# Kernel optimization log

Hardware: AMD Instinct MI355X
Metric: run time of the kernel (lower is better)

## Reference

```python
import jax, jax.numpy as jnp
import numpy as np

B, C, S = 32, 64, 112
RATIO = 8
EPS = 1e-5


def conv1x1(x, w, b):
    # 1x1 conv == channel-mixing matmul. x:[B,C,H,W], w:[O,C], b:[O]
    return jnp.einsum('oc,bchw->bohw', w, x) + b[None, :, None, None]


def dwconv(x, w, b):
    # grouped 1x1 conv with groups=C: per-channel scale + bias
    return x * w[None, :, None, None] + b[None, :, None, None]


def bn(x, g, b):
    # BatchNorm2d in training mode: batch stats over (N,H,W), biased var
    m = x.mean((0, 2, 3), keepdims=True)
    v = x.var((0, 2, 3), keepdims=True)
    return (x - m) * jax.lax.rsqrt(v + EPS) * g[None, :, None, None] + b[None, :, None, None]


def avgpool(x, k):
    # nn.AvgPool2d(k): kernel k, stride k, VALID (floor) padding
    s = jax.lax.reduce_window(x, 0.0, jax.lax.add, (1, 1, k, k), (1, 1, k, k), 'VALID')
    return s / float(k * k)


def setup_inputs() -> dict:
    key = jax.random.key(0)
    ks = jax.random.split(key, 20)
    C2, H = 2 * C, (2 * C) // RATIO

    def n(k, shape, s=0.02):
        return jax.random.normal(k, shape, jnp.float32) * s

    return {
        'rgb': jax.random.normal(ks[0], (B, C, S, S), jnp.float32),
        'fre': jax.random.normal(ks[1], (B, C, S, S), jnp.float32),
        'wq_fad': n(ks[2], (C, C)), 'bq_fad': jnp.zeros((C,), jnp.float32),
        'wq_lfs': n(ks[3], (C, C)), 'bq_lfs': jnp.zeros((C,), jnp.float32),
        'wk_fad': n(ks[4], (C, C)), 'bk_fad': jnp.zeros((C,), jnp.float32),
        'wk_lfs': n(ks[5], (C, C)), 'bk_lfs': jnp.zeros((C,), jnp.float32),
        'fad_gamma': n(ks[6], (1,), 1.0), 'lfs_gamma': n(ks[7], (1,), 1.0),
        'fad_cw': n(ks[8], (C,), 1.0), 'fad_cb': jnp.zeros((C,), jnp.float32),
        'fad_bg': jnp.ones((C,), jnp.float32), 'fad_bb': jnp.zeros((C,), jnp.float32),
        'lfs_cw': n(ks[9], (C,), 1.0), 'lfs_cb': jnp.zeros((C,), jnp.float32),
        'lfs_bg': jnp.ones((C,), jnp.float32), 'lfs_bb': jnp.zeros((C,), jnp.float32),
        'lin1_w': n(ks[10], (3,), 0.3), 'lin2_w': n(ks[11], (3,), 0.3),
        'mlp_w1': n(ks[12], (H, C2)), 'mlp_w2': n(ks[13], (C2, H)),
        'rgb_cw': n(ks[14], (C,), 1.0), 'rgb_cb': jnp.zeros((C,), jnp.float32),
        'rgb_bg': jnp.ones((C,), jnp.float32), 'rgb_bb': jnp.zeros((C,), jnp.float32),
        'fre_cw': n(ks[15], (C,), 1.0), 'fre_cb': jnp.zeros((C,), jnp.float32),
        'fre_bg': jnp.ones((C,), jnp.float32), 'fre_bb': jnp.zeros((C,), jnp.float32),
    }


def reference(rgb, fre, wq_fad, bq_fad, wq_lfs, bq_lfs, wk_fad, bk_fad, wk_lfs, bk_lfs,
              fad_gamma, lfs_gamma, fad_cw, fad_cb, fad_bg, fad_bb,
              lfs_cw, lfs_cb, lfs_bg, lfs_bb, lin1_w, lin2_w, mlp_w1, mlp_w2,
              rgb_cw, rgb_cb, rgb_bg, rgb_bb, fre_cw, fre_cb, fre_bg, fre_bb):
    Bn, Cn, Sz, _ = rgb.shape
    # ---- MixBlock: cross attention over folded (B*C) batch ----
    qF = conv1x1(rgb, wq_fad, bq_fad).reshape(Bn * Cn, Sz, Sz)
    qL = conv1x1(fre, wq_lfs, bq_lfs).reshape(Bn * Cn, Sz, Sz)
    Mq = jnp.concatenate([qF, qL], axis=2)          # [BC, S, 2S]
    kF = conv1x1(rgb, wk_fad, bk_fad).reshape(Bn * Cn, Sz, Sz).transpose(0, 2, 1)
    kL = conv1x1(fre, wk_lfs, bk_lfs).reshape(Bn * Cn, Sz, Sz).transpose(0, 2, 1)
    Mk = jnp.concatenate([kF, kL], axis=1)          # [BC, 2S, S]
    attn = jax.nn.softmax(jnp.matmul(Mq, Mk), axis=-1).reshape(Bn, Cn, Sz, Sz)
    att_lfs = fre * attn * (jax.nn.sigmoid(lfs_gamma) * 2.0 - 1.0)
    y_fad = rgb + bn(dwconv(att_lfs, fad_cw, fad_cb), fad_bg, fad_bb)
    att_fad = rgb * attn * (jax.nn.sigmoid(fad_gamma) * 2.0 - 1.0)
    y_lfs = fre + bn(dwconv(att_fad, lfs_cw, lfs_cb), lfs_bg, lfs_bb)
    # ---- MSCA on concatenated channels ----
    x = jnp.concatenate([y_fad, y_lfs], axis=1)     # [B, 2C, S, S]
    avgs, maxs = [], []
    for k in (3, 5, 7):
        m = avgpool(x, k)
        avgs.append(m.mean((2, 3)))
        maxs.append(m.max((2, 3)))
    a_p = jnp.stack(avgs, -1) @ lin1_w              # [B, 2C]
    m_p = jnp.stack(maxs, -1) @ lin2_w

    def mlp(v):
        h = jax.nn.relu(jnp.einsum('rc,bc->br', mlp_w1, v))
        return jnp.einsum('cr,br->bc', mlp_w2, h)

    ca = jax.nn.sigmoid(mlp(a_p) + mlp(m_p))        # [B, 2C]
    r_c = ca[:, :Cn, None, None]
    f_c = ca[:, Cn:, None, None]
    rgb_out = y_fad + bn(dwconv(r_c * y_fad, rgb_cw, rgb_cb), rgb_bg, rgb_bb)
    fre_out = y_lfs + bn(dwconv(f_c * y_lfs, fre_cw, fre_cb), fre_bg, fre_bb)
    return (rgb_out, fre_out)
```

## Files before the change

kernel.cpp:

```cpp
#include <hip/hip_runtime.h>
#include <hip/hip_bf16.h>
#include <stdint.h>

#define NE 25690112ull
#define PP 12544
#define SS 112
#define EPSV 1e-5f

typedef __attribute__((ext_vector_type(8))) short short8v;
typedef __attribute__((ext_vector_type(4))) float float4v;

__device__ __forceinline__ unsigned short f2bf(float x){
  union { float f; uint32_t u; } v; v.f = x;
  uint32_t r = (v.u + 0x7fffu + ((v.u >> 16) & 1u)) >> 16;
  return (unsigned short)r;
}
__device__ __forceinline__ float bf2f(unsigned short u){ return __uint_as_float(((uint32_t)u) << 16); }

__global__ __launch_bounds__(256) void k1_conv(
    const float* __restrict__ rgb, const float* __restrict__ fre,
    const float* __restrict__ wq_fad, const float* __restrict__ bq_fad,
    const float* __restrict__ wk_fad, const float* __restrict__ bk_fad,
    const float* __restrict__ wq_lfs, const float* __restrict__ bq_lfs,
    const float* __restrict__ wk_lfs, const float* __restrict__ bk_lfs,
    unsigned short* __restrict__ qF, unsigned short* __restrict__ kF,
    unsigned short* __restrict__ qL, unsigned short* __restrict__ kL)
{
  const int bx = blockIdx.x, b = blockIdx.y, z = blockIdx.z;
  const float* X  = z ? fre : rgb;
  const float* Wq = z ? wq_lfs : wq_fad;
  const float* Bq = z ? bq_lfs : bq_fad;
  const float* Wk = z ? wk_lfs : wk_fad;
  const float* Bk = z ? bk_lfs : bk_fad;
  unsigned short* Oq = z ? qL : qF;
  unsigned short* Ok = z ? kL : kF;

  const int tid = threadIdx.x, lane = tid & 63, w = tid >> 6;
  const int lc = lane & 15, l4 = lane >> 4;

  short8v wqf[4][2], wkf[4][2];
  float bq[4], bk[4];
  #pragma unroll
  for (int ot = 0; ot < 4; ++ot){
    bq[ot] = Bq[ot*16 + lc];
    bk[ot] = Bk[ot*16 + lc];
    #pragma unroll
    for (int ks = 0; ks < 2; ++ks){
      const int base = (ot*16 + lc)*64 + ks*32 + l4*8;
      const float4 q0 = *(const float4*)(Wq + base);
      const float4 q1 = *(const float4*)(Wq + base + 4);
      const float4 k0 = *(const float4*)(Wk + base);
      const float4 k1 = *(const float4*)(Wk + base + 4);
      short8v vq, vk;
      vq[0]=(short)f2bf(q0.x); vq[1]=(short)f2bf(q0.y); vq[2]=(short)f2bf(q0.z); vq[3]=(short)f2bf(q0.w);
      vq[4]=(short)f2bf(q1.x); vq[5]=(short)f2bf(q1.y); vq[6]=(short)f2bf(q1.z); vq[7]=(short)f2bf(q1.w);
      vk[0]=(short)f2bf(k0.x); vk[1]=(short)f2bf(k0.y); vk[2]=(short)f2bf(k0.z); vk[3]=(short)f2bf(k0.w);
      vk[4]=(short)f2bf(k1.x); vk[5]=(short)f2bf(k1.y); vk[6]=(short)f2bf(k1.z); vk[7]=(short)f2bf(k1.w);
      wqf[ot][ks] = vq; wkf[ot][ks] = vk;
    }
  }

  const size_t xbase = (size_t)b * 64 * PP;
  #pragma unroll
  for (int t = 0; t < 4; ++t){
    const int p0 = bx*256 + (t*4 + w)*16;
    float af[2][8];
    #pragma unroll
    for (int ks = 0; ks < 2; ++ks)
      #pragma unroll
      for (int j = 0; j < 8; ++j)
        af[ks][j] = X[xbase + (size_t)(ks*32 + l4*8 + j)*PP + p0 + lc];
    short8v a0, a1;
    #pragma unroll
    for (int j = 0; j < 8; ++j){ a0[j] = (short)f2bf(af[0][j]); a1[j] = (short)f2bf(af[1][j]); }

    float4v aq[4], ak[4];
    #pragma unroll
    for (int ot = 0; ot < 4; ++ot){
      aq[ot] = (float4v){bq[ot], bq[ot], bq[ot], bq[ot]};
      ak[ot] = (float4v){bk[ot], bk[ot], bk[ot], bk[ot]};
    }
    #pragma unroll
    for (int ot = 0; ot < 4; ++ot){
      aq[ot] = __builtin_amdgcn_mfma_f32_16x16x32_bf16(a0, wqf[ot][0], aq[ot], 0, 0, 0);
      aq[ot] = __builtin_amdgcn_mfma_f32_16x16x32_bf16(a1, wqf[ot][1], aq[ot], 0, 0, 0);
      ak[ot] = __builtin_amdgcn_mfma_f32_16x16x32_bf16(a0, wkf[ot][0], ak[ot], 0, 0, 0);
      ak[ot] = __builtin_amdgcn_mfma_f32_16x16x32_bf16(a1, wkf[ot][1], ak[ot], 0, 0, 0);
    }
    #pragma unroll
    for (int ot = 0; ot < 4; ++ot){
      const size_t off = ((size_t)b*64 + ot*16 + lc)*PP + p0 + l4*4;
      ushort4 sq, sk;
      sq.x = f2bf(aq[ot][0]); sq.y = f2bf(aq[ot][1]); sq.z = f2bf(aq[ot][2]); sq.w = f2bf(aq[ot][3]);
      sk.x = f2bf(ak[ot][0]); sk.y = f2bf(ak[ot][1]); sk.z = f2bf(ak[ot][2]); sk.w = f2bf(ak[ot][3]);
      *(ushort4*)(Oq + off) = sq;
      *(ushort4*)(Ok + off) = sk;
    }
  }
}

__global__ __launch_bounds__(448) void k2_attn(
    unsigned short* __restrict__ qF, const unsigned short* __restrict__ qL,
    const unsigned short* __restrict__ kF, const unsigned short* __restrict__ kL,
    const float* __restrict__ rgb, const float* __restrict__ fre,
    const float* __restrict__ fad_gamma, const float* __restrict__ lfs_gamma,
    float* __restrict__ stats)
{
  const int bc = blockIdx.x, c = bc & 63;
  const size_t plane = (size_t)bc * PP;
  __shared__ __align__(16) unsigned short ksF[112][128];
  __shared__ __align__(16) unsigned short ksL[112][128];
  const int tid = threadIdx.x, lane = tid & 63, w = tid >> 6;
  const int l4 = lane >> 4, lc = lane & 15;

  const uint32_t* kFu = (const uint32_t*)kF + plane/2;
  const uint32_t* kLu = (const uint32_t*)kL + plane/2;
  for (int i = tid; i < 7168; i += 448){
    int row = i >> 6, wd = i & 63;
    uint32_t vF = (wd < 56) ? kFu[row*56 + wd] : 0u;
    uint32_t vL = (wd < 56) ? kLu[row*56 + wd] : 0u;
    uint32_t byteS = (uint32_t)((row << 8) | (wd << 2)) ^ (uint32_t)((row & 7) << 4);
    *(uint32_t*)((char*)&ksF[0][0] + byteS) = vF;
    *(uint32_t*)((char*)&ksL[0][0] + byteS) = vL;
  }
  __syncthreads();

  float4v acc[7];
  #pragma unroll
  for (int ct = 0; ct < 7; ++ct) acc[ct] = (float4v)0.f;

  const unsigned short* qFp = qF + plane;
  const unsigned short* qLp = qL + plane;
  const int qrow = w*16 + lc;
  #pragma unroll
  for (int ks = 0; ks < 4; ++ks){
    short8v aF = (short8v)(short)0, aL = (short8v)(short)0;
    const int joff = ks*32 + l4*8;
    if ((ks < 3) || (l4 < 2)){
      aF = *(const short8v*)(qFp + qrow*SS + joff);
      aL = *(const short8v*)(qLp + qrow*SS + joff);
    }
    #pragma unroll
    for (int ct = 0; ct < 7; ++ct){
      uint32_t byteS = (uint32_t)((ct*16 + lc)*256 + ks*64 + l4*16) ^ (uint32_t)((lc & 7) << 4);
      short8v bF = *(const short8v*)((const char*)&ksF[0][0] + byteS);
      short8v bL = *(const short8v*)((const char*)&ksL[0][0] + byteS);
      acc[ct] = __builtin_amdgcn_mfma_f32_16x16x32_bf16(aF, bF, acc[ct], 0, 0, 0);
      acc[ct] = __builtin_amdgcn_mfma_f32_16x16x32_bf16(aL, bL, acc[ct], 0, 0, 0);
    }
  }

  const float sF = 2.f/(1.f + __expf(-fad_gamma[0])) - 1.f;
  const float sL = 2.f/(1.f + __expf(-lfs_gamma[0])) - 1.f;
  float ls1 = 0.f, lq1 = 0.f, ls2 = 0.f, lq2 = 0.f;
  unsigned short* attnP = qF + plane;

  #pragma unroll
  for (int r = 0; r < 4; ++r){
    const int i = w*16 + l4*4 + r;
    float v[7];
    #pragma unroll
    for (int ct = 0; ct < 7; ++ct) v[ct] = acc[ct][r];
    float m = fmaxf(fmaxf(fmaxf(v[0],v[1]),fmaxf(v[2],v[3])), fmaxf(fmaxf(v[4],v[5]),v[6]));
    #pragma unroll
    for (int off = 8; off; off >>= 1) m = fmaxf(m, __shfl_xor(m, off, 64));
    float e[7]; float s = 0.f;
    #pragma unroll
    for (int ct = 0; ct < 7; ++ct){ e[ct] = __expf(v[ct] - m); s += e[ct]; }
    #pragma unroll
    for (int off = 8; off; off >>= 1) s += __shfl_xor(s, off, 64);
    const float inv = 1.f / s;
    const size_t rb = plane + (size_t)i * SS;
    #pragma unroll
    for (int ct = 0; ct < 7; ++ct){
      const int col = ct*16 + lc;
      unsigned short ab = f2bf(e[ct] * inv);
      attnP[(size_t)i*SS + col] = ab;
      float a  = bf2f(ab);
      float frv = fre[rb + col], rgv = rgb[rb + col];
      float v1 = frv * a * sL, v2 = rgv * a * sF;
      ls1 += v1; lq1 += v1*v1; ls2 += v2; lq2 += v2*v2;
    }
  }
  #pragma unroll
  for (int off = 32; off; off >>= 1){
    ls1 += __shfl_xor(ls1, off, 64);
    lq1 += __shfl_xor(lq1, off, 64);
    ls2 += __shfl_xor(ls2, off, 64);
    lq2 += __shfl_xor(lq2, off, 64);
  }
  if (lane == 0){
    atomicAdd(&stats[c],       ls1);
    atomicAdd(&stats[64 + c],  lq1);
    atomicAdd(&stats[128 + c], ls2);
    atomicAdd(&stats[192 + c], lq2);
  }
}

__global__ void k3_affine1(const float* __restrict__ stats,
    const float* __restrict__ fad_cw, const float* __restrict__ fad_bg, const float* __restrict__ fad_bb,
    const float* __restrict__ lfs_cw, const float* __restrict__ lfs_bg, const float* __restrict__ lfs_bb,
    float* __restrict__ AB)
{
  int c = threadIdx.x;
  if (c >= 64) return;
  const float n = 401408.f;
  {
    float m1 = stats[c]/n, v1 = stats[64+c]/n - (stats[c]/n)*(stats[c]/n);
    float cw = fad_cw[c], g = fad_bg[c];
    float rs = rsqrtf(cw*cw*v1 + EPSV);
    AB[c]      = cw*rs*g;
    AB[64 + c] = -cw*m1*rs*g + fad_bb[c];
  }
  {
    float m2 = stats[128+c]/n, v2 = stats[192+c]/n - (stats[128+c]/n)*(stats[128+c]/n);
    float cw = lfs_cw[c], g = lfs_bg[c];
    float rs = rsqrtf(cw*cw*v2 + EPSV);
    AB[128 + c] = cw*rs*g;
    AB[192 + c] = -cw*m2*rs*g + lfs_bb[c];
  }
}

__global__ __launch_bounds__(512) void k4_fuse(
    const unsigned short* __restrict__ attn,
    const float* __restrict__ rgb, const float* __restrict__ fre,
    const float* __restrict__ AB1,
    const float* __restrict__ fad_gamma, const float* __restrict__ lfs_gamma,
    unsigned short* __restrict__ ybf, unsigned short* __restrict__ ybl,
    float* __restrict__ avgstat, float* __restrict__ maxstat,
    float4* __restrict__ planeStats)
{
  const int bc = blockIdx.x, b = bc >> 6, c = bc & 63;
  const size_t plane = (size_t)bc * PP;
  __shared__ unsigned short ys[2][112][113];
  __shared__ float redA[8][4];
  __shared__ float redS[8], redM[8];
  const int tid = threadIdx.x, lane = tid & 63, w = tid >> 6;
  const float sF = 2.f/(1.f + __expf(-fad_gamma[0])) - 1.f;
  const float sL = 2.f/(1.f + __expf(-lfs_gamma[0])) - 1.f;
  const float A1 = AB1[c], B1 = AB1[64+c], A2 = AB1[128+c], B2 = AB1[192+c];
  float s0 = 0.f, q0 = 0.f, s1 = 0.f, q1 = 0.f;

  for (int i4 = tid; i4 < 3136; i4 += 512){
    ushort4 av = *(const ushort4*)(attn + plane + (size_t)i4*4);
    float4 rg = *(const float4*)(rgb + plane + (size_t)i4*4);
    float4 fr = *(const float4*)(fre + plane + (size_t)i4*4);
    float aa[4] = {bf2f(av.x), bf2f(av.y), bf2f(av.z), bf2f(av.w)};
    float rr[4] = {rg.x, rg.y, rg.z, rg.w};
    float ff[4] = {fr.x, fr.y, fr.z, fr.w};
    float y0[4], y1[4];
    ushort4 o0, o1;
    unsigned short* p0 = &o0.x; unsigned short* p1 = &o1.x;
    #pragma unroll
    for (int j = 0; j < 4; ++j){
      float t1 = ff[j]*aa[j]*sL;
      float t2 = rr[j]*aa[j]*sF;
      y0[j] = rr[j] + A1*t1 + B1;
      y1[j] = ff[j] + A2*t2 + B2;
      s0 += y0[j]; q0 += y0[j]*y0[j];
      s1 += y1[j]; q1 += y1[j]*y1[j];
      p0[j] = f2bf(y0[j]);
      p1[j] = f2bf(y1[j]);
    }
    *(ushort4*)(ybf + plane + (size_t)i4*4) = o0;
    *(ushort4*)(ybl + plane + (size_t)i4*4) = o1;
    int r = i4 / 28, c0 = (i4 % 28) * 4;
    #pragma unroll
    for (int j = 0; j < 4; ++j){
      ys[0][r][c0+j] = p0[j];
      ys[1][r][c0+j] = p1[j];
    }
  }
  #pragma unroll
  for (int off = 32; off; off >>= 1){
    s0 += __shfl_xor(s0, off, 64); q0 += __shfl_xor(q0, off, 64);
    s1 += __shfl_xor(s1, off, 64); q1 += __shfl_xor(q1, off, 64);
  }
  if (lane == 0){ redA[w][0] = s0; redA[w][1] = q0; redA[w][2] = s1; redA[w][3] = q1; }
  __syncthreads();
  if (tid == 0){
    float a0=0,a1=0,a2=0,a3=0;
    for (int i = 0; i < 8; ++i){ a0+=redA[i][0]; a1+=redA[i][1]; a2+=redA[i][2]; a3+=redA[i][3]; }
    float4 ps = {a0,a1,a2,a3};
    planeStats[bc] = ps;
  }
  __syncthreads();

  const int kk[3] = {3,5,7};
  const int gg[3] = {37,22,16};
  for (int pl = 0; pl < 2; ++pl){
    const int cc = pl*64 + c;
    for (int ki = 0; ki < 3; ++ki){
      const int k = kk[ki], g = gg[ki];
      float sumAll = 0.f, mx = -3.0e38f;
      for (int win = tid; win < g*g; win += 512){
        int wy = win / g, wx = win % g;
        float s = 0.f;
        for (int dy = 0; dy < k; ++dy)
          for (int dx = 0; dx < k; ++dx)
            s += bf2f(ys[pl][wy*k+dy][wx*k+dx]);
        sumAll += s; mx = fmaxf(mx, s);
      }
      #pragma unroll
      for (int off = 32; off; off >>= 1){
        sumAll += __shfl_xor(sumAll, off, 64);
        mx = fmaxf(mx, __shfl_xor(mx, off, 64));
      }
      if (lane == 0){ redS[w] = sumAll; redM[w] = mx; }
      __syncthreads();
      if (tid == 0){
        float st = 0.f, mt = -3.0e38f;
        for (int i = 0; i < 8; ++i){ st += redS[i]; mt = fmaxf(mt, redM[i]); }
        int idx = (b*128 + cc)*3 + ki;
        avgstat[idx] = st / (float)(k*k*g*g);
        maxstat[idx] = mt / (float)(k*k);
      }
      __syncthreads();
    }
  }
}

__global__ void k6_mlp(const float* __restrict__ avgstat, const float* __restrict__ maxstat,
    const float* __restrict__ lin1, const float* __restrict__ lin2,
    const float* __restrict__ w1, const float* __restrict__ w2,
    float* __restrict__ ca)
{
  const int b = blockIdx.x, tid = threadIdx.x;
  __shared__ float sa[128], sm[128], hA[16], hM[16];
  int idx = (b*128 + tid)*3;
  sa[tid] = avgstat[idx]*lin1[0] + avgstat[idx+1]*lin1[1] + avgstat[idx+2]*lin1[2];
  sm[tid] = maxstat[idx]*lin2[0] + maxstat[idx+1]*lin2[1] + maxstat[idx+2]*lin2[2];
  __syncthreads();
  if (tid < 16){
    float ha = 0.f, hm = 0.f;
    for (int c2 = 0; c2 < 128; ++c2){
      ha += w1[tid*128 + c2]*sa[c2];
      hm += w1[tid*128 + c2]*sm[c2];
    }
    hA[tid] = fmaxf(ha, 0.f); hM[tid] = fmaxf(hm, 0.f);
  }
  __syncthreads();
  float o = 0.f;
  for (int r = 0; r < 16; ++r) o += w2[tid*16 + r]*(hA[r] + hM[r]);
  ca[b*128 + tid] = 1.f/(1.f + __expf(-o));
}

__global__ void k8_affineF(const float4* __restrict__ planeStats, const float* __restrict__ ca,
    const float* __restrict__ rgb_cw, const float* __restrict__ rgb_bg, const float* __restrict__ rgb_bb,
    const float* __restrict__ fre_cw, const float* __restrict__ fre_bg, const float* __restrict__ fre_bb,
    float* __restrict__ ABF)
{
  int t = threadIdx.x;
  if (t >= 128) return;
  int z = t >> 6, c = t & 63;
  float S = 0.f, Q = 0.f;
  for (int b = 0; b < 32; ++b){
    float4 ps = planeStats[b*64 + c];
    float sc = ca[b*128 + t];
    float sp = z ? ps.z : ps.x;
    float qp = z ? ps.w : ps.y;
    S += sc*sp; Q += sc*sc*qp;
  }
  const float n = 401408.f;
  float m = S/n, v = Q/n - m*m;
  float cw = z ? fre_cw[c] : rgb_cw[c];
  float g  = z ? fre_bg[c] : rgb_bg[c];
  float bb = z ? fre_bb[c] : rgb_bb[c];
  float rs = rsqrtf(cw*cw*v + EPSV);
  ABF[z*128 + c]      = cw*rs*g;
  ABF[z*128 + 64 + c] = -cw*m*rs*g + bb;
}

__global__ __launch_bounds__(256) void k9_out(
    const unsigned short* __restrict__ ybf, const unsigned short* __restrict__ ybl,
    const float* __restrict__ ca, const float* __restrict__ ABF,
    float* __restrict__ out)
{
  const int c = blockIdx.x, b = blockIdx.y, z = blockIdx.z;
  const size_t plane = ((size_t)b*64 + c)*PP;
  const unsigned short* y = z ? ybl : ybf;
  float* o = out + (z ? NE : 0) + plane;
  const float sc = ca[b*128 + z*64 + c];
  const float A = ABF[z*128 + c], Bv = ABF[z*128 + 64 + c];
  const float mul = 1.f + A*sc;
  for (int i8 = threadIdx.x; i8 < 1568; i8 += 256){
    short8v yv = *(const short8v*)(y + plane + (size_t)i8*8);
    float4 o0, o1;
    o0.x = bf2f((unsigned short)yv[0])*mul + Bv;
    o0.y = bf2f((unsigned short)yv[1])*mul + Bv;
    o0.z = bf2f((unsigned short)yv[2])*mul + Bv;
    o0.w = bf2f((unsigned short)yv[3])*mul + Bv;
    o1.x = bf2f((unsigned short)yv[4])*mul + Bv;
    o1.y = bf2f((unsigned short)yv[5])*mul + Bv;
    o1.z = bf2f((unsigned short)yv[6])*mul + Bv;
    o1.w = bf2f((unsigned short)yv[7])*mul + Bv;
    *(float4*)(&o[(size_t)i8*8])     = o0;
    *(float4*)(&o[(size_t)i8*8 + 4]) = o1;
  }
}

extern "C" void kernel_launch(void* const* d_in, const int* in_sizes, int n_in,
                              void* d_out, int out_size, void* d_ws, size_t ws_size,
                              hipStream_t stream)
{
  (void)in_sizes; (void)n_in; (void)out_size; (void)ws_size;
  const float* rgb      = (const float*)d_in[0];
  const float* fre      = (const float*)d_in[1];
  const float* wq_fad   = (const float*)d_in[2];
  const float* bq_fad   = (const float*)d_in[3];
  const float* wq_lfs   = (const float*)d_in[4];
  const float* bq_lfs   = (const float*)d_in[5];
  const float* wk_fad   = (const float*)d_in[6];
  const float* bk_fad   = (const float*)d_in[7];
  const float* wk_lfs   = (const float*)d_in[8];
  const float* bk_lfs   = (const float*)d_in[9];
  const float* fad_gamma= (const float*)d_in[10];
  const float* lfs_gamma= (const float*)d_in[11];
  const float* fad_cw   = (const float*)d_in[12];
  const float* fad_bg   = (const float*)d_in[14];
  const float* fad_bb   = (const float*)d_in[15];
  const float* lfs_cw   = (const float*)d_in[16];
  const float* lfs_bg   = (const float*)d_in[18];
  const float* lfs_bb   = (const float*)d_in[19];
  const float* lin1_w   = (const float*)d_in[20];
  const float* lin2_w   = (const float*)d_in[21];
  const float* mlp_w1   = (const float*)d_in[22];
  const float* mlp_w2   = (const float*)d_in[23];
  const float* rgb_cw   = (const float*)d_in[24];
  const float* rgb_bg   = (const float*)d_in[26];
  const float* rgb_bb   = (const float*)d_in[27];
  const float* fre_cw   = (const float*)d_in[28];
  const float* fre_bg   = (const float*)d_in[30];
  const float* fre_bb   = (const float*)d_in[31];

  char* ws = (char*)d_ws;
  unsigned short* qF = (unsigned short*)(ws);
  unsigned short* qL = (unsigned short*)(ws + 2*NE);
  unsigned short* kF = (unsigned short*)(ws + 4*NE);
  unsigned short* kL = (unsigned short*)(ws + 6*NE);
  float* sbase = (float*)(ws + 8*NE);
  float* stats      = sbase;
  float* AB1        = sbase + 256;
  float* avgstat    = sbase + 512;
  float* maxstat    = sbase + 12800;
  float* ca         = sbase + 25088;
  float* ABF        = sbase + 29184;
  float4* planeStats= (float4*)(sbase + 29440);

  hipMemsetAsync(stats, 0, 256*sizeof(float), stream);

  k1_conv<<<dim3(49,32,2), dim3(256), 0, stream>>>(rgb, fre,
      wq_fad, bq_fad, wk_fad, bk_fad, wq_lfs, bq_lfs, wk_lfs, bk_lfs,
      qF, kF, qL, kL);
  k2_attn<<<dim3(2048), dim3(448), 0, stream>>>(qF, qL, kF, kL,
      rgb, fre, fad_gamma, lfs_gamma, stats);
  k3_affine1<<<dim3(1), dim3(64), 0, stream>>>(stats,
      fad_cw, fad_bg, fad_bb, lfs_cw, lfs_bg, lfs_bb, AB1);
  k4_fuse<<<dim3(2048), dim3(512), 0, stream>>>((const unsigned short*)qF,
      rgb, fre, AB1, fad_gamma, lfs_gamma, kF, kL, avgstat, maxstat, planeStats);
  k6_mlp<<<dim3(32), dim3(128), 0, stream>>>(avgstat, maxstat,
      lin1_w, lin2_w, mlp_w1, mlp_w2, ca);
  k8_affineF<<<dim3(1), dim3(128), 0, stream>>>(planeStats, ca,
      rgb_cw, rgb_bg, rgb_bb, fre_cw, fre_bg, fre_bb, ABF);
  k9_out<<<dim3(64,32,2), dim3(256), 0, stream>>>(kF, kL, ca, ABF,
      (float*)d_out);
}
```

Measured before the change: 477.2 us.

## Stage conv input through LDS and reuse bf16 copies of rgb/fre downstream

The 1x1-conv kernel now loads its input tile with coalesced float4 reads and transposes it into swizzled LDS. MFMA operands are then read from LDS instead of from strided per-element global loads. The same kernel writes bf16 copies of rgb and fre into the output buffer, used as scratch. The attention and fuse kernels read those half-width copies instead of the fp32 inputs, cutting global read traffic at the cost of an extra write pass and bf16 rounding of the residual inputs.

```diff
diff --git a/kernel.cpp b/kernel.cpp
--- a/kernel.cpp
+++ b/kernel.cpp
@@ -24,7 +24,8 @@
     const float* __restrict__ wq_lfs, const float* __restrict__ bq_lfs,
     const float* __restrict__ wk_lfs, const float* __restrict__ bk_lfs,
     unsigned short* __restrict__ qF, unsigned short* __restrict__ kF,
-    unsigned short* __restrict__ qL, unsigned short* __restrict__ kL)
+    unsigned short* __restrict__ qL, unsigned short* __restrict__ kL,
+    unsigned short* __restrict__ rgbb, unsigned short* __restrict__ freb)
 {
   const int bx = blockIdx.x, b = blockIdx.y, z = blockIdx.z;
   const float* X  = z ? fre : rgb;
@@ -34,6 +35,9 @@
   const float* Bk = z ? bk_lfs : bk_fad;
   unsigned short* Oq = z ? qL : qF;
   unsigned short* Ok = z ? kL : kF;
+  unsigned short* Xb = z ? freb : rgbb;
+
+  __shared__ __align__(16) unsigned short xs[256 * 64];
 
   const int tid = threadIdx.x, lane = tid & 63, w = tid >> 6;
   const int lc = lane & 15, l4 = lane >> 4;
@@ -60,19 +64,44 @@
     }
   }
 
+  const int p0 = bx*256;
   const size_t xbase = (size_t)b * 64 * PP;
+  const int c0 = (tid & 15) * 4;
+  const int pq = (tid >> 4) * 4;
+  #pragma unroll
+  for (int itp = 0; itp < 4; ++itp){
+    const int p = itp*64 + pq;
+    float4 xr[4];
+    #pragma unroll
+    for (int k = 0; k < 4; ++k)
+      xr[k] = *(const float4*)(X + xbase + (size_t)(c0+k)*PP + p0 + p);
+    #pragma unroll
+    for (int k = 0; k < 4; ++k){
+      ushort4 s;
+      s.x = f2bf(xr[k].x); s.y = f2bf(xr[k].y); s.z = f2bf(xr[k].z); s.w = f2bf(xr[k].w);
+      *(ushort4*)(Xb + xbase + (size_t)(c0+k)*PP + p0 + p) = s;
+    }
+    float vals[4][4];
+    #pragma unroll
+    for (int k = 0; k < 4; ++k){ vals[k][0]=xr[k].x; vals[k][1]=xr[k].y; vals[k][2]=xr[k].z; vals[k][3]=xr[k].w; }
+    #pragma unroll
+    for (int j = 0; j < 4; ++j){
+      ushort4 t;
+      t.x = f2bf(vals[0][j]); t.y = f2bf(vals[1][j]); t.z = f2bf(vals[2][j]); t.w = f2bf(vals[3][j]);
+      uint32_t byteS = (uint32_t)((p+j)*128 + c0*2) ^ (uint32_t)(((p+j) & 7) << 4);
+      *(ushort4*)((char*)xs + byteS) = t;
+    }
+  }
+  __syncthreads();
+
   #pragma unroll
   for (int t = 0; t < 4; ++t){
-    const int p0 = bx*256 + (t*4 + w)*16;
-    float af[2][8];
-    #pragma unroll
-    for (int ks = 0; ks < 2; ++ks)
-      #pragma unroll
-      for (int j = 0; j < 8; ++j)
-        af[ks][j] = X[xbase + (size_t)(ks*32 + l4*8 + j)*PP + p0 + lc];
-    short8v a0, a1;
-    #pragma unroll
-    for (int j = 0; j < 8; ++j){ a0[j] = (short)f2bf(af[0][j]); a1[j] = (short)f2bf(af[1][j]); }
+    const int pt = (t*4 + w)*16;
+    const int row = pt + lc;
+    const uint32_t rbase = (uint32_t)(row*128) ;
+    const uint32_t sw = (uint32_t)((row & 7) << 4);
+    short8v a0 = *(const short8v*)((const char*)xs + ((rbase + l4*16) ^ sw));
+    short8v a1 = *(const short8v*)((const char*)xs + ((rbase + 64 + l4*16) ^ sw));
 
     float4v aq[4], ak[4];
     #pragma unroll
@@ -89,7 +118,7 @@
     }
     #pragma unroll
     for (int ot = 0; ot < 4; ++ot){
-      const size_t off = ((size_t)b*64 + ot*16 + lc)*PP + p0 + l4*4;
+      const size_t off = ((size_t)b*64 + ot*16 + lc)*PP + p0 + pt + l4*4;
       ushort4 sq, sk;
       sq.x = f2bf(aq[ot][0]); sq.y = f2bf(aq[ot][1]); sq.z = f2bf(aq[ot][2]); sq.w = f2bf(aq[ot][3]);
       sk.x = f2bf(ak[ot][0]); sk.y = f2bf(ak[ot][1]); sk.z = f2bf(ak[ot][2]); sk.w = f2bf(ak[ot][3]);
@@ -102,7 +131,7 @@
 __global__ __launch_bounds__(448) void k2_attn(
     unsigned short* __restrict__ qF, const unsigned short* __restrict__ qL,
     const unsigned short* __restrict__ kF, const unsigned short* __restrict__ kL,
-    const float* __restrict__ rgb, const float* __restrict__ fre,
+    const unsigned short* __restrict__ rgbb, const unsigned short* __restrict__ freb,
     const float* __restrict__ fad_gamma, const float* __restrict__ lfs_gamma,
     float* __restrict__ stats)
 {
@@ -177,7 +206,7 @@
       unsigned short ab = f2bf(e[ct] * inv);
       attnP[(size_t)i*SS + col] = ab;
       float a  = bf2f(ab);
-      float frv = fre[rb + col], rgv = rgb[rb + col];
+      float frv = bf2f(freb[rb + col]), rgv = bf2f(rgbb[rb + col]);
       float v1 = frv * a * sL, v2 = rgv * a * sF;
       ls1 += v1; lq1 += v1*v1; ls2 += v2; lq2 += v2*v2;
     }
@@ -223,7 +252,7 @@
 
 __global__ __launch_bounds__(512) void k4_fuse(
     const unsigned short* __restrict__ attn,
-    const float* __restrict__ rgb, const float* __restrict__ fre,
+    const unsigned short* __restrict__ rgbb, const unsigned short* __restrict__ freb,
     const float* __restrict__ AB1,
     const float* __restrict__ fad_gamma, const float* __restrict__ lfs_gamma,
     unsigned short* __restrict__ ybf, unsigned short* __restrict__ ybl,
@@ -243,11 +272,11 @@
 
   for (int i4 = tid; i4 < 3136; i4 += 512){
     ushort4 av = *(const ushort4*)(attn + plane + (size_t)i4*4);
-    float4 rg = *(const float4*)(rgb + plane + (size_t)i4*4);
-    float4 fr = *(const float4*)(fre + plane + (size_t)i4*4);
+    ushort4 rg = *(const ushort4*)(rgbb + plane + (size_t)i4*4);
+    ushort4 fr = *(const ushort4*)(freb + plane + (size_t)i4*4);
     float aa[4] = {bf2f(av.x), bf2f(av.y), bf2f(av.z), bf2f(av.w)};
-    float rr[4] = {rg.x, rg.y, rg.z, rg.w};
-    float ff[4] = {fr.x, fr.y, fr.z, fr.w};
+    float rr[4] = {bf2f(rg.x), bf2f(rg.y), bf2f(rg.z), bf2f(rg.w)};
+    float ff[4] = {bf2f(fr.x), bf2f(fr.y), bf2f(fr.z), bf2f(fr.w)};
     float y0[4], y1[4];
     ushort4 o0, o1;
     unsigned short* p0 = &o0.x; unsigned short* p1 = &o1.x;
@@ -446,18 +475,20 @@
   float* ca         = sbase + 25088;
   float* ABF        = sbase + 29184;
   float4* planeStats= (float4*)(sbase + 29440);
+  unsigned short* rgbb = (unsigned short*)d_out;
+  unsigned short* freb = (unsigned short*)d_out + NE;
 
   hipMemsetAsync(stats, 0, 256*sizeof(float), stream);
 
   k1_conv<<<dim3(49,32,2), dim3(256), 0, stream>>>(rgb, fre,
       wq_fad, bq_fad, wk_fad, bk_fad, wq_lfs, bq_lfs, wk_lfs, bk_lfs,
-      qF, kF, qL, kL);
+      qF, kF, qL, kL, rgbb, freb);
   k2_attn<<<dim3(2048), dim3(448), 0, stream>>>(qF, qL, kF, kL,
-      rgb, fre, fad_gamma, lfs_gamma, stats);
+      rgbb, freb, fad_gamma, lfs_gamma, stats);
   k3_affine1<<<dim3(1), dim3(64), 0, stream>>>(stats,
       fad_cw, fad_bg, fad_bb, lfs_cw, lfs_bg, lfs_bb, AB1);
   k4_fuse<<<dim3(2048), dim3(512), 0, stream>>>((const unsigned short*)qF,
-      rgb, fre, AB1, fad_gamma, lfs_gamma, kF, kL, avgstat, maxstat, planeStats);
+      rgbb, freb, AB1, fad_gamma, lfs_gamma, kF, kL, avgstat, maxstat, planeStats);
   k6_mlp<<<dim3(32), dim3(128), 0, stream>>>(avgstat, maxstat,
       lin1_w, lin2_w, mlp_w1, mlp_w2, ca);
   k8_affineF<<<dim3(1), dim3(128), 0, stream>>>(planeStats, ca,
```

Result: no change. 475.9 us (-0.3%).
